# Kernel optimization log

Hardware: AMD Instinct MI355X
Metric: run time of the kernel (lower is better)

Reference implementation:

```python
import jax, jax.numpy as jnp
import numpy as np

HID = 64   # basis_hidden_dim
NB = 8     # num_learnable_bases
N = 16     # n_super_nodes
D = 4      # latent_dim
B = 2048   # batch

_PNAMES = ["W1", "b1", "W2", "b2", "W3", "b3", "scale", "aW1", "ab1", "aW2", "ab2", "res"]


def _basis_params(key, din):
    ks = jax.random.split(key, 4)
    s = 0.1
    return [
        jax.random.normal(ks[0], (NB, din, HID)) * s, jnp.zeros((NB, HID)),
        jax.random.normal(ks[1], (NB, HID, HID)) * s, jnp.zeros((NB, HID)),
        jax.random.normal(ks[2], (NB, HID, 1)) * s, jnp.zeros((NB, 1)),
        jnp.ones((NB,)),
        jax.random.normal(ks[3], (din, HID // 2)) * s, jnp.zeros((HID // 2,)),
        jax.random.normal(jax.random.fold_in(ks[3], 1), (HID // 2, NB)) * s, jnp.zeros((NB,)),
        jnp.ones((1,)) * 0.1,
    ]


def setup_inputs() -> dict:
    key = jax.random.key(0)
    k0, k1, k2, k3, k4 = jax.random.split(key, 5)
    inp = {"z_flat": jax.random.normal(k0, (B, N * D), dtype=jnp.float32)}
    for pfx, kk, din in [("pw", k1, 8), ("nd", k2, D), ("gl", k3, N * D)]:
        for nm, v in zip(_PNAMES, _basis_params(kk, din)):
            inp[pfx + "_" + nm] = v
    ks = jax.random.split(k4, 3)
    inp["sel_W1"] = jax.random.normal(ks[0], (N * D, HID)) * 0.1
    inp["sel_b1"] = jnp.zeros((HID,))
    inp["sel_W2"] = jax.random.normal(ks[1], (HID, HID // 2)) * 0.1
    inp["sel_b2"] = jnp.zeros((HID // 2,))
    inp["sel_W3"] = jax.random.normal(ks[2], (HID // 2, 1)) * 0.1
    inp["sel_b3"] = jnp.zeros((1,))
    return inp


def _basis(x, W1, b1, W2, b2, W3, b3, scale, aW1, ab1, aW2, ab2, res):
    # x: [..., din] -> [..., 1]. NB tiny 3-layer MLPs batched over basis axis n.
    h = jax.nn.silu(jnp.einsum('...i,nih->...nh', x, W1) + b1)
    h = jax.nn.silu(jnp.einsum('...nh,nhk->...nk', h, W2) + b2)
    o = (jnp.einsum('...nh,nh->...n', h, W3[..., 0]) + b3[:, 0]) * scale  # [..., NB]
    # attention mixing over the NB basis outputs
    a = jax.nn.silu(x @ aW1 + ab1)
    a = jax.nn.softmax(a @ aW2 + ab2, axis=-1)                            # [..., NB]
    out = jnp.sum(o * a, axis=-1, keepdims=True)
    return out + res * jnp.mean(x, axis=-1, keepdims=True)                # residual


def _forward(z_flat,
             pw_W1, pw_b1, pw_W2, pw_b2, pw_W3, pw_b3, pw_scale, pw_aW1, pw_ab1, pw_aW2, pw_ab2, pw_res,
             nd_W1, nd_b1, nd_W2, nd_b2, nd_W3, nd_b3, nd_scale, nd_aW1, nd_ab1, nd_aW2, nd_ab2, nd_res,
             gl_W1, gl_b1, gl_W2, gl_b2, gl_W3, gl_b3, gl_scale, gl_aW1, gl_ab1, gl_aW2, gl_ab2, gl_res,
             sel_W1, sel_b1, sel_W2, sel_b2, sel_W3, sel_b3):
    b = z_flat.shape[0]
    z_nodes = z_flat.reshape(b, N, D)
    pos = z_nodes[:, :, :2]
    iu, ju = jnp.triu_indices(N, k=1)  # P = N*(N-1)/2 = 120 pairs
    # pairwise distances on upper-triangular pairs (no box wrap: box_size=None)
    diffs = pos[:, iu] - pos[:, ju]                     # [B, P, 2]
    d = jnp.sqrt(jnp.sum(diffs * diffs, axis=-1))       # [B, P]
    d = jnp.maximum(d, 0.001)
    inv_d = 1.0 / (d + 0.1)
    inv_sq = 1.0 / (d * d + 0.1)
    exp_d = jnp.exp(-jnp.minimum(d, 20.0))
    screened = exp_d / (d + 0.1)
    log_d = jnp.log(d + 1.0)
    # learnable pairwise basis: cat(pos_i, vel_i, pos_j, vel_j) == cat(z_i, z_j) for D=4
    pair_in = jnp.concatenate([z_nodes[:, iu], z_nodes[:, ju]], axis=-1)  # [B, P, 8]
    pw = _basis(pair_in, pw_W1, pw_b1, pw_W2, pw_b2, pw_W3, pw_b3, pw_scale,
                pw_aW1, pw_ab1, pw_aW2, pw_ab2, pw_res)[..., 0]           # [B, P]
    nd = _basis(z_nodes, nd_W1, nd_b1, nd_W2, nd_b2, nd_W3, nd_b3, nd_scale,
                nd_aW1, nd_ab1, nd_aW2, nd_ab2, nd_res)[..., 0]           # [B, N]
    gl = _basis(z_flat, gl_W1, gl_b1, gl_W2, gl_b2, gl_W3, gl_b3, gl_scale,
                gl_aW1, gl_ab1, gl_aW2, gl_ab2, gl_res)                   # [B, 1]
    X = jnp.concatenate([z_flat, d, inv_d, inv_sq, exp_d, screened, log_d, pw, nd, gl], axis=1)
    # adaptive feature selection gate
    s = jax.nn.silu(z_flat @ sel_W1 + sel_b1)
    s = jax.nn.silu(s @ sel_W2 + sel_b2)
    s = jax.nn.sigmoid(s @ sel_W3 + sel_b3)             # [B, 1]
    X = X * s
    return jnp.clip(X, -1e6, 1e6)


def reference(z_flat,
              pw_W1, pw_b1, pw_W2, pw_b2, pw_W3, pw_b3, pw_scale, pw_aW1, pw_ab1, pw_aW2, pw_ab2, pw_res,
              nd_W1, nd_b1, nd_W2, nd_b2, nd_W3, nd_b3, nd_scale, nd_aW1, nd_ab1, nd_aW2, nd_ab2, nd_res,
              gl_W1, gl_b1, gl_W2, gl_b2, gl_W3, gl_b3, gl_scale, gl_aW1, gl_ab1, gl_aW2, gl_ab2, gl_res,
              sel_W1, sel_b1, sel_W2, sel_b2, sel_W3, sel_b3):
    return _forward(z_flat,
                    pw_W1, pw_b1, pw_W2, pw_b2, pw_W3, pw_b3, pw_scale, pw_aW1, pw_ab1, pw_aW2, pw_ab2, pw_res,
                    nd_W1, nd_b1, nd_W2, nd_b2, nd_W3, nd_b3, nd_scale, nd_aW1, nd_ab1, nd_aW2, nd_ab2, nd_res,
                    gl_W1, gl_b1, gl_W2, gl_b2, gl_W3, gl_b3, gl_scale, gl_aW1, gl_ab1, gl_aW2, gl_ab2, gl_res,
                    sel_W1, sel_b1, sel_W2, sel_b2, sel_W3, sel_b3)
```

## Files before the change

kernel.cpp:

```cpp
#include <hip/hip_runtime.h>
#include <hip/hip_bf16.h>
#include <math.h>

#define XCOLS 921
#define COL_Z 0
#define COL_D 64
#define COL_INVD 184
#define COL_INVSQ 304
#define COL_EXPD 424
#define COL_SCR 544
#define COL_LOGD 664
#define COL_PW 784
#define COL_ND 904
#define COL_GL 920

#define BATCH 2048
#define NPAIRS 120
#define RPW (BATCH * NPAIRS)
#define RND (BATCH * 16)
#define RGL BATCH
#define RTOT (RPW + RND + RGL)

#define ROWS_BLK 128
#define TILES 8
#define GL_BLK 16
#define PW_BLK 1920
#define ND_BLK 256

#define WS_SGATE   0u
#define WS_ZERO    8192u
#define WS_ONE     8448u
#define WS_BW3_PW  8704u
#define WS_BW3_ND  12800u
#define WS_BW3_GL  16896u
#define WS_B1D_GL  20992u
#define WS_W1T_PW  23040u
#define WS_W1T_ND  39424u
#define WS_W1T_GL  55808u
#define WS_W2T_PW  121344u
#define WS_W2T_ND  186880u
#define WS_W2T_GL  252416u
#define WS_XF      317952u
#define WS_XGL     4774400u
#define WS_ATT     5036544u
#define WS_TAIL    14014976u

typedef unsigned short ushort_t;
typedef unsigned int uint_t;
typedef __attribute__((ext_vector_type(8))) short bf16x8;
typedef __attribute__((ext_vector_type(4))) float f32x4;

__device__ __forceinline__ float fast_rcp(float x) { return __builtin_amdgcn_rcpf(x); }
__device__ __forceinline__ float silu_f(float x) { return x * fast_rcp(1.0f + __expf(-x)); }
__device__ __forceinline__ ushort_t f2b(float f) {
    __hip_bfloat16 h = __float2bfloat16(f);
    return __builtin_bit_cast(ushort_t, h);
}
__device__ __forceinline__ uint_t pk2(float a, float b) {
    return (uint_t)f2b(a) | ((uint_t)f2b(b) << 16);
}
__device__ __forceinline__ int permS(int m) {
    return ((m >> 2) & 3) * 8 + (m & 3) + ((m >> 4) & 1) * 4 + ((m >> 5) & 1) * 32;
}

struct AArgs { const float *aW1, *ab1, *aW2, *ab2, *b3, *scale, *res; };
struct PArgs { const float *W1, *b1, *W2, *b2, *W3; };

__global__ __launch_bounds__(64) void selgeom_kernel(
    const float* __restrict__ z,
    const float* __restrict__ W1, const float* __restrict__ b1,
    const float* __restrict__ W2, const float* __restrict__ b2,
    const float* __restrict__ W3, const float* __restrict__ b3,
    float* __restrict__ s_out, float* __restrict__ out)
{
    int b = blockIdx.x;
    int t = threadIdx.x;
    __shared__ float zs[64];
    __shared__ float h1[64];
    __shared__ float h2[32];
    __shared__ float sg;
    zs[t] = z[b * 64 + t];
    __syncthreads();
    {
        float acc = b1[t];
        #pragma unroll
        for (int i = 0; i < 64; ++i) acc += zs[i] * W1[i * 64 + t];
        h1[t] = silu_f(acc);
    }
    __syncthreads();
    if (t < 32) {
        float acc = b2[t];
        #pragma unroll
        for (int i = 0; i < 64; ++i) acc += h1[i] * W2[i * 32 + t];
        h2[t] = silu_f(acc);
    }
    __syncthreads();
    if (t == 0) {
        float acc = b3[0];
        #pragma unroll
        for (int i = 0; i < 32; ++i) acc += h2[i] * W3[i];
        float s = fast_rcp(1.0f + __expf(-acc));
        sg = s;
        s_out[b] = s;
    }
    __syncthreads();
    float s = sg;
    float* row = out + (size_t)b * XCOLS;
    {
        float v = zs[t] * s;
        row[COL_Z + t] = fminf(fmaxf(v, -1e6f), 1e6f);
    }
    #pragma unroll
    for (int rep = 0; rep < 2; ++rep) {
        int p = t + rep * 64;
        if (p < NPAIRS) {
            int i = 0, pp = p;
            while (pp >= 15 - i) { pp -= 15 - i; ++i; }
            int j = i + 1 + pp;
            float dx = zs[i * 4 + 0] - zs[j * 4 + 0];
            float dy = zs[i * 4 + 1] - zs[j * 4 + 1];
            float d = sqrtf(dx * dx + dy * dy);
            d = fmaxf(d, 0.001f);
            float inv_d = fast_rcp(d + 0.1f);
            float inv_sq = fast_rcp(d * d + 0.1f);
            float exp_d = __expf(-fminf(d, 20.0f));
            float screened = exp_d * inv_d;
            float log_d = __logf(d + 1.0f);
            row[COL_D + p] = d * s;
            row[COL_INVD + p] = inv_d * s;
            row[COL_INVSQ + p] = inv_sq * s;
            row[COL_EXPD + p] = exp_d * s;
            row[COL_SCR + p] = screened * s;
            row[COL_LOGD + p] = log_d * s;
        }
    }
}

__global__ __launch_bounds__(256) void xprep_kernel(
    const float* __restrict__ z,
    AArgs apw, AArgs anda, AArgs agl,
    PArgs ppw, PArgs pnd, PArgs pgl,
    char* __restrict__ ws)
{
    const int bid = blockIdx.x;
    if (bid >= 1096) {
        int t0 = (bid - 1096) * 256 + threadIdx.x;
        const int STR = 128 * 256;
        if (t0 < 64) ((float*)(ws + WS_ZERO))[t0] = 0.f;
        if (t0 < 8) ((ushort_t*)(ws + WS_ONE))[t0] = (t0 == 0) ? f2b(1.0f) : (ushort_t)0;
        for (int t = t0; t < 16384; t += STR) {
            int which = t >> 13, u = t & 8191;
            int nn = u >> 10, m = (u >> 4) & 63, k = u & 15;
            int sm = permS(m);
            float v;
            if (which == 0)
                v = (k < 8) ? ppw.W1[nn * 512 + k * 64 + sm]
                  : (k == 8 ? ppw.b1[nn * 64 + sm] : 0.f);
            else
                v = (k < 4) ? pnd.W1[nn * 256 + k * 64 + sm]
                  : (k == 8 ? pnd.b1[nn * 64 + sm] : 0.f);
            ((ushort_t*)(ws + (which == 0 ? WS_W1T_PW : WS_W1T_ND)))[u] = f2b(v);
        }
        for (int t = t0; t < 32768; t += STR) {
            int nn = t >> 12, m = (t >> 6) & 63, k = t & 63;
            ((ushort_t*)(ws + WS_W1T_GL))[t] = f2b(pgl.W1[nn * 4096 + k * 64 + permS(m)]);
        }
        for (int t = t0; t < 512; t += STR) {
            int nn = t >> 6, m = t & 63;
            ((float*)(ws + WS_B1D_GL))[t] = pgl.b1[nn * 64 + permS(m)];
        }
        for (int t = t0; t < 3 * 32768; t += STR) {
            int which = t >> 15, u = t & 32767;
            int nn = u >> 12, kb = (u >> 9) & 7, col = (u >> 3) & 63, e = u & 7;
            int k = (kb & 3) * 8 + e + ((kb >> 2) << 5);
            const float* src = which == 0 ? ppw.W2 : which == 1 ? pnd.W2 : pgl.W2;
            ushort_t* dst = (ushort_t*)(ws + (which == 0 ? WS_W2T_PW : which == 1 ? WS_W2T_ND : WS_W2T_GL));
            dst[u] = f2b(src[nn * 4096 + k * 64 + col]);
        }
        for (int t = t0; t < 1536; t += STR) {
            int which = t >> 9, u = t & 511;
            const float* b2 = which == 0 ? ppw.b2 : which == 1 ? pnd.b2 : pgl.b2;
            const float* W3 = which == 0 ? ppw.W3 : which == 1 ? pnd.W3 : pgl.W3;
            float2* dst = (float2*)(ws + (which == 0 ? WS_BW3_PW : which == 1 ? WS_BW3_ND : WS_BW3_GL));
            dst[u] = make_float2(b2[u], W3[u]);
        }
        return;
    }

    const int urow = bid * 256 + threadIdx.x;
    const float* sg = (const float*)(ws + WS_SGATE);
    float a1acc[32];
    float mean, s;
    AArgs A;

    if (urow < RPW) {
        A = apw;
        int b = urow / 120, p = urow - b * 120;
        int i = 0, pp = p;
        while (pp >= 15 - i) { pp -= 15 - i; ++i; }
        int j = i + 1 + pp;
        const float* zb = z + b * 64;
        float4 xa = *(const float4*)(zb + i * 4);
        float4 xb = *(const float4*)(zb + j * 4);
        float x[8] = {xa.x, xa.y, xa.z, xa.w, xb.x, xb.y, xb.z, xb.w};
        uint4 xw = make_uint4(pk2(x[0], x[1]), pk2(x[2], x[3]), pk2(x[4], x[5]), pk2(x[6], x[7]));
        *(uint4*)(ws + WS_XF + (size_t)urow * 16) = xw;
        mean = (x[0] + x[1] + x[2] + x[3] + x[4] + x[5] + x[6] + x[7]) * 0.125f;
        #pragma unroll
        for (int u = 0; u < 32; ++u) {
            float acc = A.ab1[u];
            #pragma unroll
            for (int q = 0; q < 8; ++q) acc += x[q] * A.aW1[q * 32 + u];
            a1acc[u] = acc;
        }
        s = sg[b];
    } else if (urow < RPW + RND) {
        A = anda;
        int loc = urow - RPW;
        int b = loc >> 4, node = loc & 15;
        float4 xa = *(const float4*)(z + b * 64 + node * 4);
        float x[4] = {xa.x, xa.y, xa.z, xa.w};
        uint4 xw = make_uint4(pk2(x[0], x[1]), pk2(x[2], x[3]), 0u, 0u);
        *(uint4*)(ws + WS_XF + (size_t)urow * 16) = xw;
        mean = (x[0] + x[1] + x[2] + x[3]) * 0.25f;
        #pragma unroll
        for (int u = 0; u < 32; ++u) {
            float acc = A.ab1[u];
            #pragma unroll
            for (int q = 0; q < 4; ++q) acc += x[q] * A.aW1[q * 32 + u];
            a1acc[u] = acc;
        }
        s = sg[b];
    } else {
        A = agl;
        int r = urow - (RPW + RND);
        const float* zr = z + (size_t)r * 64;
        #pragma unroll
        for (int u = 0; u < 32; ++u) a1acc[u] = A.ab1[u];
        float mn = 0.f;
        #pragma unroll
        for (int c = 0; c < 8; ++c) {
            float4 f0 = *(const float4*)(zr + c * 8);
            float4 f1 = *(const float4*)(zr + c * 8 + 4);
            float xs[8] = {f0.x, f0.y, f0.z, f0.w, f1.x, f1.y, f1.z, f1.w};
            uint4 xw = make_uint4(pk2(xs[0], xs[1]), pk2(xs[2], xs[3]),
                                  pk2(xs[4], xs[5]), pk2(xs[6], xs[7]));
            *(uint4*)(ws + WS_XGL + (size_t)r * 128 + c * 16) = xw;
            #pragma unroll
            for (int q = 0; q < 8; ++q) {
                mn += xs[q];
                float xk = xs[q];
                #pragma unroll
                for (int u = 0; u < 32; ++u) a1acc[u] += xk * A.aW1[(c * 8 + q) * 32 + u];
            }
        }
        mean = mn * (1.0f / 64.0f);
        s = sg[r];
    }

    float lg[8];
    #pragma unroll
    for (int n = 0; n < 8; ++n) lg[n] = A.ab2[n];
    #pragma unroll
    for (int u = 0; u < 32; ++u) {
        float a1 = silu_f(a1acc[u]);
        #pragma unroll
        for (int n = 0; n < 8; ++n) lg[n] += a1 * A.aW2[u * 8 + n];
    }
    float m = lg[0];
    #pragma unroll
    for (int n = 1; n < 8; ++n) m = fmaxf(m, lg[n]);
    float sum = 0.f;
    #pragma unroll
    for (int n = 0; n < 8; ++n) { lg[n] = __expf(lg[n] - m); sum += lg[n]; }
    float inv = fast_rcp(sum);
    float tail = 0.f;
    float as_[8];
    #pragma unroll
    for (int n = 0; n < 8; ++n) {
        float a_n = lg[n] * inv * A.scale[n];
        tail += a_n * A.b3[n];
        as_[n] = a_n * s;
    }
    float* ag = (float*)(ws + WS_ATT) + (size_t)urow * 8;
    *(float4*)(ag + 0) = make_float4(as_[0], as_[1], as_[2], as_[3]);
    *(float4*)(ag + 4) = make_float4(as_[4], as_[5], as_[6], as_[7]);
    ((float*)(ws + WS_TAIL))[urow] = (tail + A.res[0] * mean) * s;
}

__global__ __launch_bounds__(512, 4) void basis_main_kernel(
    const char* __restrict__ ws, float* __restrict__ out)
{
    __shared__ float Att[ROWS_BLK * 9];
    __shared__ float Part[8][ROWS_BLK];
    const int tid = threadIdx.x;
    const int lane = tid & 63;
    const int n = tid >> 6;
    const int g = lane >> 4;
    const int lo = lane & 15;

    const int bid = blockIdx.x;
    int fam, rowbase, ubase;
    uint_t w1t_off, w2t_off, bw3_off;
    if (bid < GL_BLK) {
        fam = 2; rowbase = bid * ROWS_BLK; ubase = RPW + RND + rowbase;
        w1t_off = WS_W1T_GL; w2t_off = WS_W2T_GL; bw3_off = WS_BW3_GL;
    } else if (bid < GL_BLK + PW_BLK) {
        fam = 0; rowbase = (bid - GL_BLK) * ROWS_BLK; ubase = rowbase;
        w1t_off = WS_W1T_PW; w2t_off = WS_W2T_PW; bw3_off = WS_BW3_PW;
    } else {
        fam = 1; rowbase = (bid - (GL_BLK + PW_BLK)) * ROWS_BLK; ubase = RPW + rowbase;
        w1t_off = WS_W1T_ND; w2t_off = WS_W2T_ND; bw3_off = WS_BW3_ND;
    }

    {
        const float* ag = (const float*)(ws + WS_ATT) + (size_t)ubase * 8;
        #pragma unroll
        for (int q = 0; q < 2; ++q) {
            int idx = tid + q * 512;
            Att[(idx >> 3) * 9 + (idx & 7)] = ag[idx];
        }
        if (tid < ROWS_BLK) Att[tid * 9 + 8] = ((const float*)(ws + WS_TAIL))[ubase + tid];
    }

    const char* w2base = ws + w2t_off + (uint_t)(n * 8192 + g * 1024 + lo * 16);
    bf16x8 w2f0[4], w2f1[4];
    #pragma unroll
    for (int cb = 0; cb < 4; ++cb) {
        w2f0[cb] = *(const bf16x8*)(w2base + cb * 256);
        w2f1[cb] = *(const bf16x8*)(w2base + cb * 256 + 4096);
    }
    float2 bw[4];
    #pragma unroll
    for (int cb = 0; cb < 4; ++cb)
        bw[cb] = ((const float2*)(ws + bw3_off))[n * 64 + cb * 16 + lo];

    __syncthreads();

    const f32x4 zr4 = {0.f, 0.f, 0.f, 0.f};

    if (fam != 2) {
        bf16x8 af[4];
        #pragma unroll
        for (int mt = 0; mt < 4; ++mt) {
            uint_t a = (g < 2) ? (w1t_off + (uint_t)(n * 2048 + (mt * 16 + lo) * 32 + g * 16))
                               : WS_ZERO;
            af[mt] = *(const bf16x8*)(ws + a);
        }
        #pragma unroll 1
        for (int t = 0; t < TILES; ++t) {
            uint_t xoff = (g == 0) ? (WS_XF + (uint_t)(ubase + t * 16 + lo) * 16u)
                        : (g == 1) ? WS_ONE : WS_ZERO;
            bf16x8 xf = *(const bf16x8*)(ws + xoff);
            f32x4 d0 = __builtin_amdgcn_mfma_f32_16x16x32_bf16(af[0], xf, zr4, 0, 0, 0);
            f32x4 d1 = __builtin_amdgcn_mfma_f32_16x16x32_bf16(af[1], xf, zr4, 0, 0, 0);
            f32x4 d2 = __builtin_amdgcn_mfma_f32_16x16x32_bf16(af[2], xf, zr4, 0, 0, 0);
            f32x4 d3 = __builtin_amdgcn_mfma_f32_16x16x32_bf16(af[3], xf, zr4, 0, 0, 0);
            union { bf16x8 v; uint_t u[4]; } A0, A1;
            A0.u[0] = pk2(silu_f(d0[0]), silu_f(d0[1]));
            A0.u[1] = pk2(silu_f(d0[2]), silu_f(d0[3]));
            A0.u[2] = pk2(silu_f(d1[0]), silu_f(d1[1]));
            A0.u[3] = pk2(silu_f(d1[2]), silu_f(d1[3]));
            A1.u[0] = pk2(silu_f(d2[0]), silu_f(d2[1]));
            A1.u[1] = pk2(silu_f(d2[2]), silu_f(d2[3]));
            A1.u[2] = pk2(silu_f(d3[0]), silu_f(d3[1]));
            A1.u[3] = pk2(silu_f(d3[2]), silu_f(d3[3]));
            float pv0 = 0.f, pv1 = 0.f, pv2 = 0.f, pv3 = 0.f;
            #pragma unroll
            for (int cb = 0; cb < 4; ++cb) {
                f32x4 acc = __builtin_amdgcn_mfma_f32_16x16x32_bf16(A0.v, w2f0[cb], zr4, 0, 0, 0);
                acc = __builtin_amdgcn_mfma_f32_16x16x32_bf16(A1.v, w2f1[cb], acc, 0, 0, 0);
                pv0 += silu_f(acc[0] + bw[cb].x) * bw[cb].y;
                pv1 += silu_f(acc[1] + bw[cb].x) * bw[cb].y;
                pv2 += silu_f(acc[2] + bw[cb].x) * bw[cb].y;
                pv3 += silu_f(acc[3] + bw[cb].x) * bw[cb].y;
            }
            float pvv[4] = {pv0, pv1, pv2, pv3};
            #pragma unroll
            for (int r = 0; r < 4; ++r) {
                float v = pvv[r];
                v += __shfl_xor(v, 1);
                v += __shfl_xor(v, 2);
                v += __shfl_xor(v, 4);
                v += __shfl_xor(v, 8);
                if (lo == 0) {
                    int row = t * 16 + g * 4 + r;
                    Part[n][row] = Att[row * 9 + n] * v;
                }
            }
        }
    } else {
        float4 b1r[4];
        #pragma unroll
        for (int mt = 0; mt < 4; ++mt)
            b1r[mt] = *(const float4*)(ws + WS_B1D_GL + (uint_t)(n * 64 + mt * 16 + g * 4) * 4u);
        const char* w1b = ws + w1t_off + (uint_t)(n * 8192 + g * 16 + lo * 128);
        #pragma unroll 1
        for (int t = 0; t < TILES; ++t) {
            const char* xg = ws + WS_XGL + (size_t)(rowbase + t * 16 + lo) * 128;
            bf16x8 xf0 = *(const bf16x8*)(xg + g * 16);
            bf16x8 xf1 = *(const bf16x8*)(xg + 64 + g * 16);
            f32x4 d0 = __builtin_amdgcn_mfma_f32_16x16x32_bf16(*(const bf16x8*)(w1b + 0), xf0, zr4, 0, 0, 0);
            d0 = __builtin_amdgcn_mfma_f32_16x16x32_bf16(*(const bf16x8*)(w1b + 64), xf1, d0, 0, 0, 0);
            f32x4 d1 = __builtin_amdgcn_mfma_f32_16x16x32_bf16(*(const bf16x8*)(w1b + 2048), xf0, zr4, 0, 0, 0);
            d1 = __builtin_amdgcn_mfma_f32_16x16x32_bf16(*(const bf16x8*)(w1b + 2112), xf1, d1, 0, 0, 0);
            f32x4 d2 = __builtin_amdgcn_mfma_f32_16x16x32_bf16(*(const bf16x8*)(w1b + 4096), xf0, zr4, 0, 0, 0);
            d2 = __builtin_amdgcn_mfma_f32_16x16x32_bf16(*(const bf16x8*)(w1b + 4160), xf1, d2, 0, 0, 0);
            f32x4 d3 = __builtin_amdgcn_mfma_f32_16x16x32_bf16(*(const bf16x8*)(w1b + 6144), xf0, zr4, 0, 0, 0);
            d3 = __builtin_amdgcn_mfma_f32_16x16x32_bf16(*(const bf16x8*)(w1b + 6208), xf1, d3, 0, 0, 0);
            union { bf16x8 v; uint_t u[4]; } A0, A1;
            A0.u[0] = pk2(silu_f(d0[0] + b1r[0].x), silu_f(d0[1] + b1r[0].y));
            A0.u[1] = pk2(silu_f(d0[2] + b1r[0].z), silu_f(d0[3] + b1r[0].w));
            A0.u[2] = pk2(silu_f(d1[0] + b1r[1].x), silu_f(d1[1] + b1r[1].y));
            A0.u[3] = pk2(silu_f(d1[2] + b1r[1].z), silu_f(d1[3] + b1r[1].w));
            A1.u[0] = pk2(silu_f(d2[0] + b1r[2].x), silu_f(d2[1] + b1r[2].y));
            A1.u[1] = pk2(silu_f(d2[2] + b1r[2].z), silu_f(d2[3] + b1r[2].w));
            A1.u[2] = pk2(silu_f(d3[0] + b1r[3].x), silu_f(d3[1] + b1r[3].y));
            A1.u[3] = pk2(silu_f(d3[2] + b1r[3].z), silu_f(d3[3] + b1r[3].w));
            float pv0 = 0.f, pv1 = 0.f, pv2 = 0.f, pv3 = 0.f;
            #pragma unroll
            for (int cb = 0; cb < 4; ++cb) {
                f32x4 acc = __builtin_amdgcn_mfma_f32_16x16x32_bf16(A0.v, w2f0[cb], zr4, 0, 0, 0);
                acc = __builtin_amdgcn_mfma_f32_16x16x32_bf16(A1.v, w2f1[cb], acc, 0, 0, 0);
                pv0 += silu_f(acc[0] + bw[cb].x) * bw[cb].y;
                pv1 += silu_f(acc[1] + bw[cb].x) * bw[cb].y;
                pv2 += silu_f(acc[2] + bw[cb].x) * bw[cb].y;
                pv3 += silu_f(acc[3] + bw[cb].x) * bw[cb].y;
            }
            float pvv[4] = {pv0, pv1, pv2, pv3};
            #pragma unroll
            for (int r = 0; r < 4; ++r) {
                float v = pvv[r];
                v += __shfl_xor(v, 1);
                v += __shfl_xor(v, 2);
                v += __shfl_xor(v, 4);
                v += __shfl_xor(v, 8);
                if (lo == 0) {
                    int row = t * 16 + g * 4 + r;
                    Part[n][row] = Att[row * 9 + n] * v;
                }
            }
        }
    }

    __syncthreads();

    if (tid < ROWS_BLK) {
        float v = Att[tid * 9 + 8];
        #pragma unroll
        for (int w = 0; w < 8; ++w) v += Part[w][tid];
        v = fminf(fmaxf(v, -1e6f), 1e6f);
        int rg = rowbase + tid;
        int bb, colo;
        if (fam == 0) { bb = rg / 120; colo = COL_PW + (rg - bb * 120); }
        else if (fam == 1) { bb = rg >> 4; colo = COL_ND + (rg & 15); }
        else { bb = rg; colo = COL_GL; }
        out[(size_t)bb * XCOLS + colo] = v;
    }
}

extern "C" void kernel_launch(void* const* d_in, const int* in_sizes, int n_in,
                              void* d_out, int out_size, void* d_ws, size_t ws_size,
                              hipStream_t stream) {
    const float* z = (const float*)d_in[0];
    const float* pw[12]; const float* nd[12]; const float* gl[12];
    for (int i = 0; i < 12; ++i) pw[i] = (const float*)d_in[1 + i];
    for (int i = 0; i < 12; ++i) nd[i] = (const float*)d_in[13 + i];
    for (int i = 0; i < 12; ++i) gl[i] = (const float*)d_in[25 + i];
    const float* sel_W1 = (const float*)d_in[37];
    const float* sel_b1 = (const float*)d_in[38];
    const float* sel_W2 = (const float*)d_in[39];
    const float* sel_b2 = (const float*)d_in[40];
    const float* sel_W3 = (const float*)d_in[41];
    const float* sel_b3 = (const float*)d_in[42];

    float* out = (float*)d_out;
    char* ws = (char*)d_ws;

    selgeom_kernel<<<BATCH, 64, 0, stream>>>(
        z, sel_W1, sel_b1, sel_W2, sel_b2, sel_W3, sel_b3,
        (float*)(ws + WS_SGATE), out);

    AArgs apw = {pw[7], pw[8], pw[9], pw[10], pw[5], pw[6], pw[11]};
    AArgs anda = {nd[7], nd[8], nd[9], nd[10], nd[5], nd[6], nd[11]};
    AArgs agl = {gl[7], gl[8], gl[9], gl[10], gl[5], gl[6], gl[11]};
    PArgs ppw = {pw[0], pw[1], pw[2], pw[3], pw[4]};
    PArgs pnd = {nd[0], nd[1], nd[2], nd[3], nd[4]};
    PArgs pgl = {gl[0], gl[1], gl[2], gl[3], gl[4]};

    xprep_kernel<<<1096 + 128, 256, 0, stream>>>(z, apw, anda, agl, ppw, pnd, pgl, ws);

    basis_main_kernel<<<GL_BLK + PW_BLK + ND_BLK, 512, 0, stream>>>(ws, out);
}
```

Baseline: 128.0 us.

## Fuse selection-gate kernel into prep kernel and defer gate scaling to final store

Merges the selection-gate/geometry kernel into the attention/weight prep kernel as extra blocks that each handle four batch rows, so one launch goes away. Removing the dependency on the gate lets the prep kernel write unscaled attention and tail values. The main kernel now reads the gate per output row and applies it at the final store. It also raises the main kernel's launch_bounds occupancy hint from 4 to 8, which may force register spilling.

```diff
diff --git a/kernel.cpp b/kernel.cpp
--- a/kernel.cpp
+++ b/kernel.cpp
@@ -26,6 +26,10 @@
 #define GL_BLK 16
 #define PW_BLK 1920
 #define ND_BLK 256
+
+#define PREP_SG   512
+#define PREP_ROW  1096
+#define PREP_WP   128
 
 #define WS_SGATE   0u
 #define WS_ZERO    8192u
@@ -65,87 +69,86 @@
 
 struct AArgs { const float *aW1, *ab1, *aW2, *ab2, *b3, *scale, *res; };
 struct PArgs { const float *W1, *b1, *W2, *b2, *W3; };
-
-__global__ __launch_bounds__(64) void selgeom_kernel(
+struct SArgs { const float *W1, *b1, *W2, *b2, *W3, *b3; };
+
+__global__ __launch_bounds__(256) void prep_all_kernel(
     const float* __restrict__ z,
-    const float* __restrict__ W1, const float* __restrict__ b1,
-    const float* __restrict__ W2, const float* __restrict__ b2,
-    const float* __restrict__ W3, const float* __restrict__ b3,
-    float* __restrict__ s_out, float* __restrict__ out)
-{
-    int b = blockIdx.x;
-    int t = threadIdx.x;
-    __shared__ float zs[64];
-    __shared__ float h1[64];
-    __shared__ float h2[32];
-    __shared__ float sg;
-    zs[t] = z[b * 64 + t];
-    __syncthreads();
-    {
-        float acc = b1[t];
-        #pragma unroll
-        for (int i = 0; i < 64; ++i) acc += zs[i] * W1[i * 64 + t];
-        h1[t] = silu_f(acc);
-    }
-    __syncthreads();
-    if (t < 32) {
-        float acc = b2[t];
-        #pragma unroll
-        for (int i = 0; i < 64; ++i) acc += h1[i] * W2[i * 32 + t];
-        h2[t] = silu_f(acc);
-    }
-    __syncthreads();
-    if (t == 0) {
-        float acc = b3[0];
-        #pragma unroll
-        for (int i = 0; i < 32; ++i) acc += h2[i] * W3[i];
-        float s = fast_rcp(1.0f + __expf(-acc));
-        sg = s;
-        s_out[b] = s;
-    }
-    __syncthreads();
-    float s = sg;
-    float* row = out + (size_t)b * XCOLS;
-    {
-        float v = zs[t] * s;
-        row[COL_Z + t] = fminf(fmaxf(v, -1e6f), 1e6f);
-    }
-    #pragma unroll
-    for (int rep = 0; rep < 2; ++rep) {
-        int p = t + rep * 64;
-        if (p < NPAIRS) {
-            int i = 0, pp = p;
-            while (pp >= 15 - i) { pp -= 15 - i; ++i; }
-            int j = i + 1 + pp;
-            float dx = zs[i * 4 + 0] - zs[j * 4 + 0];
-            float dy = zs[i * 4 + 1] - zs[j * 4 + 1];
-            float d = sqrtf(dx * dx + dy * dy);
-            d = fmaxf(d, 0.001f);
-            float inv_d = fast_rcp(d + 0.1f);
-            float inv_sq = fast_rcp(d * d + 0.1f);
-            float exp_d = __expf(-fminf(d, 20.0f));
-            float screened = exp_d * inv_d;
-            float log_d = __logf(d + 1.0f);
-            row[COL_D + p] = d * s;
-            row[COL_INVD + p] = inv_d * s;
-            row[COL_INVSQ + p] = inv_sq * s;
-            row[COL_EXPD + p] = exp_d * s;
-            row[COL_SCR + p] = screened * s;
-            row[COL_LOGD + p] = log_d * s;
-        }
-    }
-}
-
-__global__ __launch_bounds__(256) void xprep_kernel(
-    const float* __restrict__ z,
+    SArgs sel,
     AArgs apw, AArgs anda, AArgs agl,
     PArgs ppw, PArgs pnd, PArgs pgl,
-    char* __restrict__ ws)
+    char* __restrict__ ws, float* __restrict__ out)
 {
     const int bid = blockIdx.x;
-    if (bid >= 1096) {
-        int t0 = (bid - 1096) * 256 + threadIdx.x;
-        const int STR = 128 * 256;
+    const int tid = threadIdx.x;
+
+    if (bid < PREP_SG) {
+        __shared__ float zs[4][64];
+        __shared__ float h1[4][64];
+        __shared__ float h2s[4][32];
+        __shared__ float sgv[4];
+        const int grp = tid >> 6, tl = tid & 63;
+        const int b = bid * 4 + grp;
+        zs[grp][tl] = z[b * 64 + tl];
+        __syncthreads();
+        {
+            float acc = sel.b1[tl];
+            #pragma unroll
+            for (int i = 0; i < 64; ++i) acc += zs[grp][i] * sel.W1[i * 64 + tl];
+            h1[grp][tl] = silu_f(acc);
+        }
+        __syncthreads();
+        if (tl < 32) {
+            float acc = sel.b2[tl];
+            #pragma unroll
+            for (int i = 0; i < 64; ++i) acc += h1[grp][i] * sel.W2[i * 32 + tl];
+            h2s[grp][tl] = silu_f(acc);
+        }
+        __syncthreads();
+        if (tl == 0) {
+            float acc = sel.b3[0];
+            #pragma unroll
+            for (int i = 0; i < 32; ++i) acc += h2s[grp][i] * sel.W3[i];
+            float s = fast_rcp(1.0f + __expf(-acc));
+            sgv[grp] = s;
+            ((float*)(ws + WS_SGATE))[b] = s;
+        }
+        __syncthreads();
+        float s = sgv[grp];
+        float* row = out + (size_t)b * XCOLS;
+        {
+            float v = zs[grp][tl] * s;
+            row[COL_Z + tl] = fminf(fmaxf(v, -1e6f), 1e6f);
+        }
+        #pragma unroll
+        for (int rep = 0; rep < 2; ++rep) {
+            int p = tl + rep * 64;
+            if (p < NPAIRS) {
+                int i = 0, pp = p;
+                while (pp >= 15 - i) { pp -= 15 - i; ++i; }
+                int j = i + 1 + pp;
+                float dx = zs[grp][i * 4 + 0] - zs[grp][j * 4 + 0];
+                float dy = zs[grp][i * 4 + 1] - zs[grp][j * 4 + 1];
+                float d = sqrtf(dx * dx + dy * dy);
+                d = fmaxf(d, 0.001f);
+                float inv_d = fast_rcp(d + 0.1f);
+                float inv_sq = fast_rcp(d * d + 0.1f);
+                float exp_d = __expf(-fminf(d, 20.0f));
+                float screened = exp_d * inv_d;
+                float log_d = __logf(d + 1.0f);
+                row[COL_D + p] = d * s;
+                row[COL_INVD + p] = inv_d * s;
+                row[COL_INVSQ + p] = inv_sq * s;
+                row[COL_EXPD + p] = exp_d * s;
+                row[COL_SCR + p] = screened * s;
+                row[COL_LOGD + p] = log_d * s;
+            }
+        }
+        return;
+    }
+
+    if (bid >= PREP_SG + PREP_ROW) {
+        int t0 = (bid - (PREP_SG + PREP_ROW)) * 256 + tid;
+        const int STR = PREP_WP * 256;
         if (t0 < 64) ((float*)(ws + WS_ZERO))[t0] = 0.f;
         if (t0 < 8) ((ushort_t*)(ws + WS_ONE))[t0] = (t0 == 0) ? f2b(1.0f) : (ushort_t)0;
         for (int t = t0; t < 16384; t += STR) {
@@ -187,10 +190,9 @@
         return;
     }
 
-    const int urow = bid * 256 + threadIdx.x;
-    const float* sg = (const float*)(ws + WS_SGATE);
+    const int urow = (bid - PREP_SG) * 256 + tid;
     float a1acc[32];
-    float mean, s;
+    float mean;
     AArgs A;
 
     if (urow < RPW) {
@@ -213,7 +215,6 @@
             for (int q = 0; q < 8; ++q) acc += x[q] * A.aW1[q * 32 + u];
             a1acc[u] = acc;
         }
-        s = sg[b];
     } else if (urow < RPW + RND) {
         A = anda;
         int loc = urow - RPW;
@@ -230,7 +231,6 @@
             for (int q = 0; q < 4; ++q) acc += x[q] * A.aW1[q * 32 + u];
             a1acc[u] = acc;
         }
-        s = sg[b];
     } else {
         A = agl;
         int r = urow - (RPW + RND);
@@ -255,7 +255,6 @@
             }
         }
         mean = mn * (1.0f / 64.0f);
-        s = sg[r];
     }
 
     float lg[8];
@@ -280,15 +279,15 @@
     for (int n = 0; n < 8; ++n) {
         float a_n = lg[n] * inv * A.scale[n];
         tail += a_n * A.b3[n];
-        as_[n] = a_n * s;
+        as_[n] = a_n;
     }
     float* ag = (float*)(ws + WS_ATT) + (size_t)urow * 8;
     *(float4*)(ag + 0) = make_float4(as_[0], as_[1], as_[2], as_[3]);
     *(float4*)(ag + 4) = make_float4(as_[4], as_[5], as_[6], as_[7]);
-    ((float*)(ws + WS_TAIL))[urow] = (tail + A.res[0] * mean) * s;
-}
-
-__global__ __launch_bounds__(512, 4) void basis_main_kernel(
+    ((float*)(ws + WS_TAIL))[urow] = tail + A.res[0] * mean;
+}
+
+__global__ __launch_bounds__(512, 8) void basis_main_kernel(
     const char* __restrict__ ws, float* __restrict__ out)
 {
     __shared__ float Att[ROWS_BLK * 9];
@@ -311,6 +310,16 @@
     } else {
         fam = 1; rowbase = (bid - (GL_BLK + PW_BLK)) * ROWS_BLK; ubase = RPW + rowbase;
         w1t_off = WS_W1T_ND; w2t_off = WS_W2T_ND; bw3_off = WS_BW3_ND;
+    }
+
+    int st_bb = 0, st_colo = 0;
+    float st_s = 0.f;
+    if (tid < ROWS_BLK) {
+        int rg = rowbase + tid;
+        if (fam == 0) { st_bb = rg / 120; st_colo = COL_PW + (rg - st_bb * 120); }
+        else if (fam == 1) { st_bb = rg >> 4; st_colo = COL_ND + (rg & 15); }
+        else { st_bb = rg; st_colo = COL_GL; }
+        st_s = ((const float*)(ws + WS_SGATE))[st_bb];
     }
 
     {
@@ -449,13 +458,9 @@
         float v = Att[tid * 9 + 8];
         #pragma unroll
         for (int w = 0; w < 8; ++w) v += Part[w][tid];
+        v *= st_s;
         v = fminf(fmaxf(v, -1e6f), 1e6f);
-        int rg = rowbase + tid;
-        int bb, colo;
-        if (fam == 0) { bb = rg / 120; colo = COL_PW + (rg - bb * 120); }
-        else if (fam == 1) { bb = rg >> 4; colo = COL_ND + (rg & 15); }
-        else { bb = rg; colo = COL_GL; }
-        out[(size_t)bb * XCOLS + colo] = v;
+        out[(size_t)st_bb * XCOLS + st_colo] = v;
     }
 }
 
@@ -467,19 +472,12 @@
     for (int i = 0; i < 12; ++i) pw[i] = (const float*)d_in[1 + i];
     for (int i = 0; i < 12; ++i) nd[i] = (const float*)d_in[13 + i];
     for (int i = 0; i < 12; ++i) gl[i] = (const float*)d_in[25 + i];
-    const float* sel_W1 = (const float*)d_in[37];
-    const float* sel_b1 = (const float*)d_in[38];
-    const float* sel_W2 = (const float*)d_in[39];
-    const float* sel_b2 = (const float*)d_in[40];
-    const float* sel_W3 = (const float*)d_in[41];
-    const float* sel_b3 = (const float*)d_in[42];
+
+    SArgs sel = {(const float*)d_in[37], (const float*)d_in[38], (const float*)d_in[39],
+                 (const float*)d_in[40], (const float*)d_in[41], (const float*)d_in[42]};
 
     float* out = (float*)d_out;
     char* ws = (char*)d_ws;
-
-    selgeom_kernel<<<BATCH, 64, 0, stream>>>(
-        z, sel_W1, sel_b1, sel_W2, sel_b2, sel_W3, sel_b3,
-        (float*)(ws + WS_SGATE), out);
 
     AArgs apw = {pw[7], pw[8], pw[9], pw[10], pw[5], pw[6], pw[11]};
     AArgs anda = {nd[7], nd[8], nd[9], nd[10], nd[5], nd[6], nd[11]};
@@ -488,7 +486,8 @@
     PArgs pnd = {nd[0], nd[1], nd[2], nd[3], nd[4]};
     PArgs pgl = {gl[0], gl[1], gl[2], gl[3], gl[4]};
 
-    xprep_kernel<<<1096 + 128, 256, 0, stream>>>(z, apw, anda, agl, ppw, pnd, pgl, ws);
+    prep_all_kernel<<<PREP_SG + PREP_ROW + PREP_WP, 256, 0, stream>>>(
+        z, sel, apw, anda, agl, ppw, pnd, pgl, ws, out);
 
     basis_main_kernel<<<GL_BLK + PW_BLK + ND_BLK, 512, 0, stream>>>(ws, out);
 }
```

Result: slower. 221.8 us (+73.3%).
